# Kernel optimization log

Measured on AMD Instinct MI355X. Metric: run time of the kernel, lower is better.

## Reference

```python
import jax, jax.numpy as jnp
import numpy as np

COORD_DIM, PARAM_DIM, H, L, O = 3, 8, 128, 5, 5
B, N_PTS = 16, 50000


def setup_inputs() -> dict:
    key = jax.random.key(0)
    ks = jax.random.split(key, 16)
    def w(k, shape, fan_in):
        return jax.random.normal(k, shape, dtype=jnp.float32) / np.sqrt(fan_in)
    inp = {
        "coords": jax.random.normal(ks[0], (B, N_PTS, COORD_DIM), dtype=jnp.float32),
        "params": jax.random.normal(ks[1], (B, PARAM_DIM), dtype=jnp.float32),
        # branch MLP: param_dim -> H (x5 hidden, rowdy tanh) -> H*O
        "branch_W0": w(ks[2], (PARAM_DIM, H), PARAM_DIM),
        "branch_b0": jnp.zeros((H,), jnp.float32),
        "branch_Wh": w(ks[3], (L - 1, H, H), H),
        "branch_bh": jnp.zeros((L - 1, H), jnp.float32),
        "branch_alpha": jnp.ones((L, H), jnp.float32),
        "branch_Wf": w(ks[4], (H, H * O), H),
        "branch_bf": jnp.zeros((H * O,), jnp.float32),
        # trunk: coord_dim -> H (x5, FiLM by branch cumsum, rowdy tanh) -> H
        "trunk_W0": w(ks[5], (COORD_DIM, H), COORD_DIM),
        "trunk_b0": jnp.zeros((H,), jnp.float32),
        "trunk_Wh": w(ks[6], (L - 1, H, H), H),
        "trunk_bh": jnp.zeros((L - 1, H), jnp.float32),
        "trunk_alpha": jnp.ones((L, H), jnp.float32),
        "trunk_Wf": w(ks[7], (H, H), H),
        "trunk_bf": jnp.zeros((H,), jnp.float32),
    }
    return inp


def reference(coords, params, branch_W0, branch_b0, branch_Wh, branch_bh,
              branch_alpha, branch_Wf, branch_bf, trunk_W0, trunk_b0,
              trunk_Wh, trunk_bh, trunk_alpha, trunk_Wf, trunk_bf):
    # ---- branch MLP with RowdyActivation, keeping hidden outputs ----
    h = branch_alpha[0] * jnp.tanh(params @ branch_W0 + branch_b0)  # (B,H)
    hiddens = [h]
    for i in range(L - 1):
        h = branch_alpha[i + 1] * jnp.tanh(h @ branch_Wh[i] + branch_bh[i])
        hiddens.append(h)
    branch_out = h @ branch_Wf + branch_bf  # (B, H*O)
    # cumulative sums S_i = sum_{j<=i} hidden_j
    S = [hiddens[0]]
    for i in range(1, L):
        S.append(hiddens[i] + S[-1])
    # ---- trunk with FiLM modulation ----
    x = coords @ trunk_W0 + trunk_b0                       # (B,n,H)
    x = trunk_alpha[0] * jnp.tanh(x * S[0][:, None, :])
    for i in range(1, L):
        x = x @ trunk_Wh[i - 1] + trunk_bh[i - 1]
        x = trunk_alpha[i] * jnp.tanh(x * S[i][:, None, :])
    YL = x @ trunk_Wf + trunk_bf                           # (B,n,H)
    ZL = branch_out.reshape(B, O, H)                       # (B,O,H)
    # out[b,n,o] = sum_h ZL[b,o,h] * YL[b,n,h]  (tiled matmul, no (B,n,O,H) temp)
    return jnp.einsum('bnh,boh->bno', YL, ZL)
```

## Files before the change

kernel.cpp:

```cpp
#include <hip/hip_runtime.h>
#include <math.h>

#define H      128
#define LNUM   5
#define ONUM   5
#define BATCH  16
#define NPTS   50000
#define TP     128
#define XROW   152

#define K2LOG2E 2.8853900817779268f

typedef _Float16      half8    __attribute__((ext_vector_type(8)));
typedef float         floatx4  __attribute__((ext_vector_type(4)));
typedef unsigned int  uint2v   __attribute__((ext_vector_type(2)));
typedef unsigned int  uint4v   __attribute__((ext_vector_type(4)));
typedef unsigned short ushort8_t __attribute__((ext_vector_type(8)));

static __device__ __forceinline__ unsigned short f2h(float f) {
    _Float16 h = (_Float16)f;
    return __builtin_bit_cast(unsigned short, h);
}
static __device__ __forceinline__ unsigned int packh(float a, float b) {
    return (unsigned int)f2h(a) | ((unsigned int)f2h(b) << 16);
}

__global__ __launch_bounds__(512)
void fold_kernel(const float* __restrict__ params,
                 const float* __restrict__ bW0, const float* __restrict__ bb0,
                 const float* __restrict__ bWh, const float* __restrict__ bbh,
                 const float* __restrict__ balpha,
                 const float* __restrict__ bWf, const float* __restrict__ bbf,
                 const float* __restrict__ tW0, const float* __restrict__ tb0,
                 const float* __restrict__ tWh, const float* __restrict__ tbh,
                 const float* __restrict__ tWf, const float* __restrict__ talpha,
                 const float* __restrict__ tbf,
                 unsigned short* __restrict__ w0s, unsigned short* __restrict__ whs,
                 unsigned short* __restrict__ wcomb, float* __restrict__ bcomb,
                 float* __restrict__ binit) {
    const int b = blockIdx.x, l = blockIdx.y, t = threadIdx.x;
    __shared__ float hbuf[H];
    __shared__ float Sneed[H];
    __shared__ float pbuf[8];
    __shared__ float zl_sh[ONUM][H];
    if (t < 8) pbuf[t] = params[b * 8 + t];
    __syncthreads();

    float scum = 0.0f;
    if (t < H) {
        float acc = bb0[t];
        for (int k = 0; k < 8; ++k) acc += pbuf[k] * bW0[k * H + t];
        float h = balpha[t] * tanhf(acc);
        hbuf[t] = h;
        scum = h;
        if (l == 0) Sneed[t] = scum;
    }
    for (int i = 1; i < LNUM; ++i) {
        __syncthreads();
        float hn = 0.0f;
        if (t < H) {
            const float* Wl = bWh + (i - 1) * H * H;
            float a2 = bbh[(i - 1) * H + t];
            for (int k = 0; k < H; ++k) a2 += hbuf[k] * Wl[k * H + t];
            hn = balpha[i * H + t] * tanhf(a2);
        }
        __syncthreads();
        if (t < H) {
            hbuf[t] = hn;
            scum += hn;
            if (i == l) Sneed[t] = scum;
        }
    }
    __syncthreads();

    if (l == 5) {
        for (int idx = t; idx < ONUM * H; idx += 512) {
            int o = idx >> 7, hh = idx & 127;
            float z = bbf[o * H + hh];
            for (int k = 0; k < H; ++k) z += hbuf[k] * bWf[k * (H * ONUM) + o * H + hh];
            zl_sh[o][hh] = z;
        }
        __syncthreads();
        for (int j = t; j < 16 * H; j += 512) {
            int o = j >> 7, f = j & 127;
            float v = 0.0f;
            if (o < ONUM) {
                const float* wfr = tWf + f * H;
                float s = 0.0f;
                for (int h = 0; h < H; ++h) s += wfr[h] * zl_sh[o][h];
                v = talpha[4 * H + f] * s;
            }
            wcomb[b * 16 * H + j] = f2h(v);
        }
        if (t < 16) {
            float v = 0.0f;
            if (t < ONUM)
                for (int h = 0; h < H; ++h) v += tbf[h] * zl_sh[t][h];
            bcomb[b * 16 + t] = v;
        }
    } else if (l == 0) {
        if (t < H) binit[(b * LNUM + 0) * H + t] = K2LOG2E * Sneed[t] * tb0[t];
        unsigned int* dst = (unsigned int*)(w0s + b * H * 32);
        for (int j = t; j < H * 16; j += 512) {
            int f = j >> 4, k0 = (j & 15) << 1;
            float s = K2LOG2E * Sneed[f];
            float v0 = (k0 < 3)     ? s * tW0[k0 * H + f]       : 0.0f;
            float v1 = (k0 + 1 < 3) ? s * tW0[(k0 + 1) * H + f] : 0.0f;
            dst[j] = packh(v0, v1);
        }
    } else {
        if (t < H) binit[(b * LNUM + l) * H + t] = K2LOG2E * Sneed[t] * tbh[(l - 1) * H + t];
        const float* Wsrc = tWh + (l - 1) * H * H;
        unsigned int* dst = (unsigned int*)(whs + (b * 4 + (l - 1)) * H * H);
        for (int j = t; j < H * H / 2; j += 512) {
            int f = j >> 6, k0 = (j & 63) << 1;
            float s = K2LOG2E * Sneed[f];
            dst[j] = packh(s * Wsrc[k0 * H + f] * talpha[(l - 1) * H + k0],
                           s * Wsrc[(k0 + 1) * H + f] * talpha[(l - 1) * H + k0 + 1]);
        }
    }
}

__global__ __launch_bounds__(256, 3)
void trunk_kernel(const float* __restrict__ coords,
                  const unsigned short* __restrict__ w0s,
                  const unsigned short* __restrict__ whs,
                  const float* __restrict__ binit,
                  const unsigned short* __restrict__ wcomb,
                  const float* __restrict__ bcomb,
                  float* __restrict__ out) {
    const int b    = blockIdx.y;
    const int n0   = blockIdx.x * TP;
    const int tid  = threadIdx.x;
    const int lane = tid & 63;
    const int w    = tid >> 6;
    const int q    = lane >> 4;
    const int c    = lane & 15;
    const int mq   = w * 32;

    __shared__ unsigned short xs[TP * XROW];

    int valid = NPTS - n0; if (valid > TP) valid = TP;
    {
        int p = tid >> 1, hh = tid & 1;
        if (hh == 0) {
            float c0 = 0.f, c1 = 0.f, c2 = 0.f;
            if (p < valid) {
                const float* cp = coords + ((size_t)b * NPTS + n0 + p) * 3;
                c0 = cp[0]; c1 = cp[1]; c2 = cp[2];
            }
            uint4v z;
            z.x = __builtin_bit_cast(unsigned int, __builtin_amdgcn_cvt_pkrtz(c0, c1));
            z.y = __builtin_bit_cast(unsigned int, __builtin_amdgcn_cvt_pkrtz(c2, 0.0f));
            z.z = 0; z.w = 0;
            *(uint4v*)&xs[p * XROW + 0] = z;
            uint4v zz = {0, 0, 0, 0};
            *(uint4v*)&xs[p * XROW + 8] = zz;
        } else {
            uint4v zz = {0, 0, 0, 0};
            *(uint4v*)&xs[p * XROW + 16] = zz;
            *(uint4v*)&xs[p * XROW + 24] = zz;
        }
    }
    __syncthreads();

    floatx4 acc[2][8];

    #pragma unroll
    for (int mt = 0; mt < 2; ++mt) {
        floatx4 bi4 = *(const floatx4*)&binit[(b * LNUM + 0) * H + mq + mt * 16 + q * 4];
        #pragma unroll
        for (int nt = 0; nt < 8; ++nt) acc[mt][nt] = bi4;
    }
    {
        const unsigned short* w0b = w0s + b * H * 32;
        half8 af[2];
        #pragma unroll
        for (int mt = 0; mt < 2; ++mt)
            af[mt] = __builtin_bit_cast(half8,
                *(const ushort8_t*)&w0b[(mq + mt * 16 + c) * 32 + q * 8]);
        #pragma unroll
        for (int nt = 0; nt < 8; ++nt) {
            half8 bfr = __builtin_bit_cast(half8,
                *(const ushort8_t*)&xs[(nt * 16 + c) * XROW + q * 8]);
            #pragma unroll
            for (int mt = 0; mt < 2; ++mt)
                acc[mt][nt] = __builtin_amdgcn_mfma_f32_16x16x32_f16(af[mt], bfr, acc[mt][nt], 0, 0, 0);
        }
    }
    __syncthreads();
    #pragma unroll
    for (int mt = 0; mt < 2; ++mt) {
        int f0 = mq + mt * 16 + q * 4;
        #pragma unroll
        for (int nt = 0; nt < 8; ++nt) {
            int pt = nt * 16 + c;
            floatx4 v = acc[mt][nt];
            #pragma unroll
            for (int r = 0; r < 4; ++r) {
                float e  = __builtin_amdgcn_exp2f(v[r]);
                float rc = __builtin_amdgcn_rcpf(e + 1.0f);
                v[r] = __builtin_fmaf(-2.0f, rc, 1.0f);
            }
            uint2v u;
            u.x = __builtin_bit_cast(unsigned int, __builtin_amdgcn_cvt_pkrtz(v[0], v[1]));
            u.y = __builtin_bit_cast(unsigned int, __builtin_amdgcn_cvt_pkrtz(v[2], v[3]));
            *(uint2v*)&xs[pt * XROW + f0] = u;
        }
    }

    for (int l = 1; l <= 4; ++l) {
        const unsigned short* wl = whs + (b * 4 + (l - 1)) * H * H;
        #pragma unroll
        for (int mt = 0; mt < 2; ++mt) {
            floatx4 bi4 = *(const floatx4*)&binit[(b * LNUM + l) * H + mq + mt * 16 + q * 4];
            #pragma unroll
            for (int nt = 0; nt < 8; ++nt) acc[mt][nt] = bi4;
        }
        __syncthreads();
        #pragma unroll
        for (int s = 0; s < 4; ++s) {
            half8 af[2];
            #pragma unroll
            for (int mt = 0; mt < 2; ++mt)
                af[mt] = __builtin_bit_cast(half8,
                    *(const ushort8_t*)&wl[(mq + mt * 16 + c) * H + s * 32 + q * 8]);
            #pragma unroll
            for (int nt = 0; nt < 8; ++nt) {
                half8 bfr = __builtin_bit_cast(half8,
                    *(const ushort8_t*)&xs[(nt * 16 + c) * XROW + s * 32 + q * 8]);
                #pragma unroll
                for (int mt = 0; mt < 2; ++mt)
                    acc[mt][nt] = __builtin_amdgcn_mfma_f32_16x16x32_f16(af[mt], bfr, acc[mt][nt], 0, 0, 0);
            }
        }
        __syncthreads();
        #pragma unroll
        for (int mt = 0; mt < 2; ++mt) {
            int f0 = mq + mt * 16 + q * 4;
            #pragma unroll
            for (int nt = 0; nt < 8; ++nt) {
                int pt = nt * 16 + c;
                floatx4 v = acc[mt][nt];
                #pragma unroll
                for (int r = 0; r < 4; ++r) {
                    float e  = __builtin_amdgcn_exp2f(v[r]);
                    float rc = __builtin_amdgcn_rcpf(e + 1.0f);
                    v[r] = __builtin_fmaf(-2.0f, rc, 1.0f);
                }
                uint2v u;
                u.x = __builtin_bit_cast(unsigned int, __builtin_amdgcn_cvt_pkrtz(v[0], v[1]));
                u.y = __builtin_bit_cast(unsigned int, __builtin_amdgcn_cvt_pkrtz(v[2], v[3]));
                *(uint2v*)&xs[pt * XROW + f0] = u;
            }
        }
    }
    __syncthreads();

    {
        floatx4 bc = *(const floatx4*)&bcomb[b * 16 + q * 4];
        floatx4 oacc[2] = {bc, bc};
        const unsigned short* wc = wcomb + b * 16 * H;
        #pragma unroll
        for (int s = 0; s < 4; ++s) {
            half8 af = __builtin_bit_cast(half8,
                *(const ushort8_t*)&wc[c * H + s * 32 + q * 8]);
            #pragma unroll
            for (int nt = 0; nt < 2; ++nt) {
                half8 bfr = __builtin_bit_cast(half8,
                    *(const ushort8_t*)&xs[(w * 32 + nt * 16 + c) * XROW + s * 32 + q * 8]);
                oacc[nt] = __builtin_amdgcn_mfma_f32_16x16x32_f16(af, bfr, oacc[nt], 0, 0, 0);
            }
        }
        #pragma unroll
        for (int nt = 0; nt < 2; ++nt) {
            int pt = n0 + w * 32 + nt * 16 + c;
            if (pt < NPTS) {
                float* op = out + ((size_t)b * NPTS + pt) * ONUM;
                if (q == 0) {
                    op[0] = oacc[nt][0]; op[1] = oacc[nt][1];
                    op[2] = oacc[nt][2]; op[3] = oacc[nt][3];
                } else if (q == 1) {
                    op[4] = oacc[nt][0];
                }
            }
        }
    }
}

extern "C" void kernel_launch(void* const* d_in, const int* in_sizes, int n_in,
                              void* d_out, int out_size, void* d_ws, size_t ws_size,
                              hipStream_t stream) {
    const float* coords       = (const float*)d_in[0];
    const float* params       = (const float*)d_in[1];
    const float* branch_W0    = (const float*)d_in[2];
    const float* branch_b0    = (const float*)d_in[3];
    const float* branch_Wh    = (const float*)d_in[4];
    const float* branch_bh    = (const float*)d_in[5];
    const float* branch_alpha = (const float*)d_in[6];
    const float* branch_Wf    = (const float*)d_in[7];
    const float* branch_bf    = (const float*)d_in[8];
    const float* trunk_W0     = (const float*)d_in[9];
    const float* trunk_b0     = (const float*)d_in[10];
    const float* trunk_Wh     = (const float*)d_in[11];
    const float* trunk_bh     = (const float*)d_in[12];
    const float* trunk_alpha  = (const float*)d_in[13];
    const float* trunk_Wf     = (const float*)d_in[14];
    const float* trunk_bf     = (const float*)d_in[15];
    float* out = (float*)d_out;

    char* ws = (char*)d_ws;
    float*          binit = (float*)(ws + 0);
    unsigned short* wcomb = (unsigned short*)(ws + 40960);
    float*          bcomb = (float*)(ws + 106496);
    unsigned short* w0s   = (unsigned short*)(ws + 107520);
    unsigned short* whs   = (unsigned short*)(ws + 238592);

    fold_kernel<<<dim3(BATCH, 6), 512, 0, stream>>>(params, branch_W0, branch_b0,
                                                    branch_Wh, branch_bh, branch_alpha,
                                                    branch_Wf, branch_bf,
                                                    trunk_W0, trunk_b0, trunk_Wh, trunk_bh,
                                                    trunk_Wf, trunk_alpha, trunk_bf,
                                                    w0s, whs, wcomb, bcomb, binit);
    trunk_kernel<<<dim3((NPTS + TP - 1) / TP, BATCH), 256, 0, stream>>>(
        coords, w0s, whs, binit, wcomb, bcomb, out);
}
```

Before: 287.2 us.

## Split point tile into two halves and overlap MFMA with tanh epilogue

The 128-point tile is split into two 64-point halves with separate accumulator sets. While one half's MFMA layer runs, the other half's tanh epilogue and fp16 writeback run in the same instruction stream. The intent is to overlap transcendental ALU work with matrix-core work, and to fold the bias into the first MFMA. This costs the same register count but adds more barriers per layer and may change the instruction schedule or register pressure.

```diff
diff --git a/kernel.cpp b/kernel.cpp
--- a/kernel.cpp
+++ b/kernel.cpp
@@ -164,83 +164,16 @@
     }
     __syncthreads();
 
-    floatx4 acc[2][8];
-
-    #pragma unroll
-    for (int mt = 0; mt < 2; ++mt) {
-        floatx4 bi4 = *(const floatx4*)&binit[(b * LNUM + 0) * H + mq + mt * 16 + q * 4];
-        #pragma unroll
-        for (int nt = 0; nt < 8; ++nt) acc[mt][nt] = bi4;
-    }
-    {
-        const unsigned short* w0b = w0s + b * H * 32;
-        half8 af[2];
-        #pragma unroll
-        for (int mt = 0; mt < 2; ++mt)
-            af[mt] = __builtin_bit_cast(half8,
-                *(const ushort8_t*)&w0b[(mq + mt * 16 + c) * 32 + q * 8]);
-        #pragma unroll
-        for (int nt = 0; nt < 8; ++nt) {
-            half8 bfr = __builtin_bit_cast(half8,
-                *(const ushort8_t*)&xs[(nt * 16 + c) * XROW + q * 8]);
-            #pragma unroll
-            for (int mt = 0; mt < 2; ++mt)
-                acc[mt][nt] = __builtin_amdgcn_mfma_f32_16x16x32_f16(af[mt], bfr, acc[mt][nt], 0, 0, 0);
-        }
-    }
-    __syncthreads();
-    #pragma unroll
-    for (int mt = 0; mt < 2; ++mt) {
-        int f0 = mq + mt * 16 + q * 4;
-        #pragma unroll
-        for (int nt = 0; nt < 8; ++nt) {
-            int pt = nt * 16 + c;
-            floatx4 v = acc[mt][nt];
-            #pragma unroll
-            for (int r = 0; r < 4; ++r) {
-                float e  = __builtin_amdgcn_exp2f(v[r]);
-                float rc = __builtin_amdgcn_rcpf(e + 1.0f);
-                v[r] = __builtin_fmaf(-2.0f, rc, 1.0f);
-            }
-            uint2v u;
-            u.x = __builtin_bit_cast(unsigned int, __builtin_amdgcn_cvt_pkrtz(v[0], v[1]));
-            u.y = __builtin_bit_cast(unsigned int, __builtin_amdgcn_cvt_pkrtz(v[2], v[3]));
-            *(uint2v*)&xs[pt * XROW + f0] = u;
-        }
-    }
-
-    for (int l = 1; l <= 4; ++l) {
-        const unsigned short* wl = whs + (b * 4 + (l - 1)) * H * H;
-        #pragma unroll
-        for (int mt = 0; mt < 2; ++mt) {
-            floatx4 bi4 = *(const floatx4*)&binit[(b * LNUM + l) * H + mq + mt * 16 + q * 4];
-            #pragma unroll
-            for (int nt = 0; nt < 8; ++nt) acc[mt][nt] = bi4;
-        }
-        __syncthreads();
-        #pragma unroll
-        for (int s = 0; s < 4; ++s) {
-            half8 af[2];
-            #pragma unroll
-            for (int mt = 0; mt < 2; ++mt)
-                af[mt] = __builtin_bit_cast(half8,
-                    *(const ushort8_t*)&wl[(mq + mt * 16 + c) * H + s * 32 + q * 8]);
-            #pragma unroll
-            for (int nt = 0; nt < 8; ++nt) {
-                half8 bfr = __builtin_bit_cast(half8,
-                    *(const ushort8_t*)&xs[(nt * 16 + c) * XROW + s * 32 + q * 8]);
-                #pragma unroll
-                for (int mt = 0; mt < 2; ++mt)
-                    acc[mt][nt] = __builtin_amdgcn_mfma_f32_16x16x32_f16(af[mt], bfr, acc[mt][nt], 0, 0, 0);
-            }
-        }
-        __syncthreads();
+    floatx4 accA[2][4];
+    floatx4 accB[2][4];
+
+    auto epi = [&](int h, floatx4 (&acc)[2][4]) {
         #pragma unroll
         for (int mt = 0; mt < 2; ++mt) {
             int f0 = mq + mt * 16 + q * 4;
             #pragma unroll
-            for (int nt = 0; nt < 8; ++nt) {
-                int pt = nt * 16 + c;
+            for (int nt = 0; nt < 4; ++nt) {
+                int pt = h * 64 + nt * 16 + c;
                 floatx4 v = acc[mt][nt];
                 #pragma unroll
                 for (int r = 0; r < 4; ++r) {
@@ -254,7 +187,100 @@
                 *(uint2v*)&xs[pt * XROW + f0] = u;
             }
         }
-    }
+    };
+
+    {
+        const float* bi0 = &binit[(b * LNUM + 0) * H];
+        const unsigned short* w0b = w0s + b * H * 32;
+        half8 af[2];
+        floatx4 bi4[2];
+        #pragma unroll
+        for (int mt = 0; mt < 2; ++mt) {
+            af[mt] = __builtin_bit_cast(half8,
+                *(const ushort8_t*)&w0b[(mq + mt * 16 + c) * 32 + q * 8]);
+            bi4[mt] = *(const floatx4*)&bi0[mq + mt * 16 + q * 4];
+        }
+        #pragma unroll
+        for (int nt = 0; nt < 4; ++nt) {
+            half8 bfr = __builtin_bit_cast(half8,
+                *(const ushort8_t*)&xs[(nt * 16 + c) * XROW + q * 8]);
+            #pragma unroll
+            for (int mt = 0; mt < 2; ++mt)
+                accA[mt][nt] = __builtin_amdgcn_mfma_f32_16x16x32_f16(af[mt], bfr, bi4[mt], 0, 0, 0);
+        }
+        #pragma unroll
+        for (int nt = 0; nt < 4; ++nt) {
+            half8 bfr = __builtin_bit_cast(half8,
+                *(const ushort8_t*)&xs[(64 + nt * 16 + c) * XROW + q * 8]);
+            #pragma unroll
+            for (int mt = 0; mt < 2; ++mt)
+                accB[mt][nt] = __builtin_amdgcn_mfma_f32_16x16x32_f16(af[mt], bfr, bi4[mt], 0, 0, 0);
+        }
+    }
+    __syncthreads();
+    epi(0, accA);
+    __syncthreads();
+
+    #pragma unroll
+    for (int l = 1; l <= 4; ++l) {
+        const unsigned short* wl = whs + (b * 4 + (l - 1)) * H * H;
+        const float* bi = &binit[(b * LNUM + l) * H];
+
+        {
+            #pragma unroll
+            for (int mt = 0; mt < 2; ++mt) {
+                floatx4 bi4 = *(const floatx4*)&bi[mq + mt * 16 + q * 4];
+                #pragma unroll
+                for (int nt = 0; nt < 4; ++nt) accA[mt][nt] = bi4;
+            }
+            #pragma unroll
+            for (int s = 0; s < 4; ++s) {
+                half8 af[2];
+                #pragma unroll
+                for (int mt = 0; mt < 2; ++mt)
+                    af[mt] = __builtin_bit_cast(half8,
+                        *(const ushort8_t*)&wl[(mq + mt * 16 + c) * H + s * 32 + q * 8]);
+                #pragma unroll
+                for (int nt = 0; nt < 4; ++nt) {
+                    half8 bfr = __builtin_bit_cast(half8,
+                        *(const ushort8_t*)&xs[(nt * 16 + c) * XROW + s * 32 + q * 8]);
+                    #pragma unroll
+                    for (int mt = 0; mt < 2; ++mt)
+                        accA[mt][nt] = __builtin_amdgcn_mfma_f32_16x16x32_f16(af[mt], bfr, accA[mt][nt], 0, 0, 0);
+                }
+            }
+            epi(1, accB);
+        }
+        __syncthreads();
+
+        {
+            #pragma unroll
+            for (int mt = 0; mt < 2; ++mt) {
+                floatx4 bi4 = *(const floatx4*)&bi[mq + mt * 16 + q * 4];
+                #pragma unroll
+                for (int nt = 0; nt < 4; ++nt) accB[mt][nt] = bi4;
+            }
+            #pragma unroll
+            for (int s = 0; s < 4; ++s) {
+                half8 af[2];
+                #pragma unroll
+                for (int mt = 0; mt < 2; ++mt)
+                    af[mt] = __builtin_bit_cast(half8,
+                        *(const ushort8_t*)&wl[(mq + mt * 16 + c) * H + s * 32 + q * 8]);
+                #pragma unroll
+                for (int nt = 0; nt < 4; ++nt) {
+                    half8 bfr = __builtin_bit_cast(half8,
+                        *(const ushort8_t*)&xs[(64 + nt * 16 + c) * XROW + s * 32 + q * 8]);
+                    #pragma unroll
+                    for (int mt = 0; mt < 2; ++mt)
+                        accB[mt][nt] = __builtin_amdgcn_mfma_f32_16x16x32_f16(af[mt], bfr, accB[mt][nt], 0, 0, 0);
+                }
+            }
+            epi(0, accA);
+        }
+        __syncthreads();
+    }
+    epi(1, accB);
     __syncthreads();
 
     {
```

Measured after the change: 342.9 us. 1.19x slower.

## Repartition trunk MLP so each wave owns its own point rows, removing block barriers

Applied to the files above, without the earlier changes.

Each wave now computes all 128 features for its own 32 points, instead of 32 features for all 128 points of the tile. Every wave then reads and writes only its own rows of the shared activation buffer, so all __syncthreads between layers are removed. This also cuts the B-fragment LDS reads per MFMA step and folds the bias into the first MFMA. The trade-off is that every wave now fetches the full weight matrices from global/L2 rather than a quarter of them, which quadruples per-block weight traffic and may expose load latency.

```diff
diff --git a/kernel.cpp b/kernel.cpp
--- a/kernel.cpp
+++ b/kernel.cpp
@@ -129,20 +129,20 @@
                   const unsigned short* __restrict__ wcomb,
                   const float* __restrict__ bcomb,
                   float* __restrict__ out) {
-    const int b    = blockIdx.y;
-    const int n0   = blockIdx.x * TP;
-    const int tid  = threadIdx.x;
-    const int lane = tid & 63;
-    const int w    = tid >> 6;
-    const int q    = lane >> 4;
-    const int c    = lane & 15;
-    const int mq   = w * 32;
+    const int b     = blockIdx.y;
+    const int n0    = blockIdx.x * TP;
+    const int tid   = threadIdx.x;
+    const int lane  = tid & 63;
+    const int w     = tid >> 6;
+    const int q     = lane >> 4;
+    const int c     = lane & 15;
+    const int pbase = w * 32;
 
     __shared__ unsigned short xs[TP * XROW];
 
     int valid = NPTS - n0; if (valid > TP) valid = TP;
     {
-        int p = tid >> 1, hh = tid & 1;
+        int p = pbase + (lane >> 1), hh = lane & 1;
         if (hh == 0) {
             float c0 = 0.f, c1 = 0.f, c2 = 0.f;
             if (p < valid) {
@@ -162,85 +162,16 @@
             *(uint4v*)&xs[p * XROW + 24] = zz;
         }
     }
-    __syncthreads();
-
-    floatx4 acc[2][8];
-
-    #pragma unroll
-    for (int mt = 0; mt < 2; ++mt) {
-        floatx4 bi4 = *(const floatx4*)&binit[(b * LNUM + 0) * H + mq + mt * 16 + q * 4];
-        #pragma unroll
-        for (int nt = 0; nt < 8; ++nt) acc[mt][nt] = bi4;
-    }
-    {
-        const unsigned short* w0b = w0s + b * H * 32;
-        half8 af[2];
-        #pragma unroll
-        for (int mt = 0; mt < 2; ++mt)
-            af[mt] = __builtin_bit_cast(half8,
-                *(const ushort8_t*)&w0b[(mq + mt * 16 + c) * 32 + q * 8]);
-        #pragma unroll
-        for (int nt = 0; nt < 8; ++nt) {
-            half8 bfr = __builtin_bit_cast(half8,
-                *(const ushort8_t*)&xs[(nt * 16 + c) * XROW + q * 8]);
+
+    floatx4 acc[8][2];
+
+    auto epi = [&]() {
+        #pragma unroll
+        for (int mt = 0; mt < 8; ++mt) {
+            int f0 = mt * 16 + q * 4;
             #pragma unroll
-            for (int mt = 0; mt < 2; ++mt)
-                acc[mt][nt] = __builtin_amdgcn_mfma_f32_16x16x32_f16(af[mt], bfr, acc[mt][nt], 0, 0, 0);
-        }
-    }
-    __syncthreads();
-    #pragma unroll
-    for (int mt = 0; mt < 2; ++mt) {
-        int f0 = mq + mt * 16 + q * 4;
-        #pragma unroll
-        for (int nt = 0; nt < 8; ++nt) {
-            int pt = nt * 16 + c;
-            floatx4 v = acc[mt][nt];
-            #pragma unroll
-            for (int r = 0; r < 4; ++r) {
-                float e  = __builtin_amdgcn_exp2f(v[r]);
-                float rc = __builtin_amdgcn_rcpf(e + 1.0f);
-                v[r] = __builtin_fmaf(-2.0f, rc, 1.0f);
-            }
-            uint2v u;
-            u.x = __builtin_bit_cast(unsigned int, __builtin_amdgcn_cvt_pkrtz(v[0], v[1]));
-            u.y = __builtin_bit_cast(unsigned int, __builtin_amdgcn_cvt_pkrtz(v[2], v[3]));
-            *(uint2v*)&xs[pt * XROW + f0] = u;
-        }
-    }
-
-    for (int l = 1; l <= 4; ++l) {
-        const unsigned short* wl = whs + (b * 4 + (l - 1)) * H * H;
-        #pragma unroll
-        for (int mt = 0; mt < 2; ++mt) {
-            floatx4 bi4 = *(const floatx4*)&binit[(b * LNUM + l) * H + mq + mt * 16 + q * 4];
-            #pragma unroll
-            for (int nt = 0; nt < 8; ++nt) acc[mt][nt] = bi4;
-        }
-        __syncthreads();
-        #pragma unroll
-        for (int s = 0; s < 4; ++s) {
-            half8 af[2];
-            #pragma unroll
-            for (int mt = 0; mt < 2; ++mt)
-                af[mt] = __builtin_bit_cast(half8,
-                    *(const ushort8_t*)&wl[(mq + mt * 16 + c) * H + s * 32 + q * 8]);
-            #pragma unroll
-            for (int nt = 0; nt < 8; ++nt) {
-                half8 bfr = __builtin_bit_cast(half8,
-                    *(const ushort8_t*)&xs[(nt * 16 + c) * XROW + s * 32 + q * 8]);
-                #pragma unroll
-                for (int mt = 0; mt < 2; ++mt)
-                    acc[mt][nt] = __builtin_amdgcn_mfma_f32_16x16x32_f16(af[mt], bfr, acc[mt][nt], 0, 0, 0);
-            }
-        }
-        __syncthreads();
-        #pragma unroll
-        for (int mt = 0; mt < 2; ++mt) {
-            int f0 = mq + mt * 16 + q * 4;
-            #pragma unroll
-            for (int nt = 0; nt < 8; ++nt) {
-                int pt = nt * 16 + c;
+            for (int nt = 0; nt < 2; ++nt) {
+                int pt = pbase + nt * 16 + c;
                 floatx4 v = acc[mt][nt];
                 #pragma unroll
                 for (int r = 0; r < 4; ++r) {
@@ -254,8 +185,54 @@
                 *(uint2v*)&xs[pt * XROW + f0] = u;
             }
         }
-    }
-    __syncthreads();
+    };
+
+    {
+        const float* bi0 = &binit[(b * LNUM + 0) * H];
+        const unsigned short* w0b = w0s + b * H * 32;
+        half8 bfr[2];
+        #pragma unroll
+        for (int nt = 0; nt < 2; ++nt)
+            bfr[nt] = __builtin_bit_cast(half8,
+                *(const ushort8_t*)&xs[(pbase + nt * 16 + c) * XROW + q * 8]);
+        #pragma unroll
+        for (int mt = 0; mt < 8; ++mt) {
+            half8 af = __builtin_bit_cast(half8,
+                *(const ushort8_t*)&w0b[(mt * 16 + c) * 32 + q * 8]);
+            floatx4 bi4 = *(const floatx4*)&bi0[mt * 16 + q * 4];
+            acc[mt][0] = __builtin_amdgcn_mfma_f32_16x16x32_f16(af, bfr[0], bi4, 0, 0, 0);
+            acc[mt][1] = __builtin_amdgcn_mfma_f32_16x16x32_f16(af, bfr[1], bi4, 0, 0, 0);
+        }
+    }
+    epi();
+
+    #pragma unroll
+    for (int l = 1; l <= 4; ++l) {
+        const unsigned short* wl = whs + (b * 4 + (l - 1)) * H * H;
+        const float* bi = &binit[(b * LNUM + l) * H];
+        #pragma unroll
+        for (int mt = 0; mt < 8; ++mt) {
+            floatx4 bi4 = *(const floatx4*)&bi[mt * 16 + q * 4];
+            acc[mt][0] = bi4;
+            acc[mt][1] = bi4;
+        }
+        #pragma unroll
+        for (int s = 0; s < 4; ++s) {
+            half8 bfr[2];
+            #pragma unroll
+            for (int nt = 0; nt < 2; ++nt)
+                bfr[nt] = __builtin_bit_cast(half8,
+                    *(const ushort8_t*)&xs[(pbase + nt * 16 + c) * XROW + s * 32 + q * 8]);
+            #pragma unroll
+            for (int mt = 0; mt < 8; ++mt) {
+                half8 af = __builtin_bit_cast(half8,
+                    *(const ushort8_t*)&wl[(mt * 16 + c) * H + s * 32 + q * 8]);
+                acc[mt][0] = __builtin_amdgcn_mfma_f32_16x16x32_f16(af, bfr[0], acc[mt][0], 0, 0, 0);
+                acc[mt][1] = __builtin_amdgcn_mfma_f32_16x16x32_f16(af, bfr[1], acc[mt][1], 0, 0, 0);
+            }
+        }
+        epi();
+    }
 
     {
         floatx4 bc = *(const floatx4*)&bcomb[b * 16 + q * 4];
@@ -268,13 +245,13 @@
             #pragma unroll
             for (int nt = 0; nt < 2; ++nt) {
                 half8 bfr = __builtin_bit_cast(half8,
-                    *(const ushort8_t*)&xs[(w * 32 + nt * 16 + c) * XROW + s * 32 + q * 8]);
+                    *(const ushort8_t*)&xs[(pbase + nt * 16 + c) * XROW + s * 32 + q * 8]);
                 oacc[nt] = __builtin_amdgcn_mfma_f32_16x16x32_f16(af, bfr, oacc[nt], 0, 0, 0);
             }
         }
         #pragma unroll
         for (int nt = 0; nt < 2; ++nt) {
-            int pt = n0 + w * 32 + nt * 16 + c;
+            int pt = n0 + pbase + nt * 16 + c;
             if (pt < NPTS) {
                 float* op = out + ((size_t)b * NPTS + pt) * ONUM;
                 if (q == 0) {
```

Measured after the change: 562.9 us. 96.0% more time.
